# Optimization experiments

Measured on AMD Instinct MI355X. Metric: run time of the kernel, lower is better.

The kernel has to match this reference:

```python
import jax, jax.numpy as jnp
import numpy as np

B, S, K, N = 8, 8192, 1024, 1024  # batch, seq, in_features, out_features

def setup_inputs() -> dict:
    key = jax.random.key(0)
    k1, k2, k3, k4 = jax.random.split(key, 4)
    x = jax.random.normal(k1, (B, S, K), dtype=jnp.float32)
    # int8 codes stored as float (matches fp16 CB parameter in the module)
    CB = jnp.clip(jnp.round(jax.random.normal(k2, (N, K), dtype=jnp.float32) * 42.0), -127.0, 127.0)
    # per-output-channel absmax scales (positive)
    SCB = jax.random.uniform(k3, (N,), dtype=jnp.float32, minval=0.5, maxval=2.0)
    bias = jax.random.normal(k4, (N,), dtype=jnp.float32) * 0.02
    return {"x": x, "CB": CB, "SCB": SCB, "bias": bias}

def reference(x, CB, SCB, bias):
    # out = linear(x, CB) * (SCB/127) + bias  -- scale applied AFTER the GEMM,
    # exactly as in the non-BFA forward path of my_8bit_linear.
    out = jnp.einsum('bsk,nk->bsn', x, CB)        # [B, S, N]
    out = out * (SCB * (1.0 / 127.0)) + bias      # per-output-channel dequant + bias
    return out
```

## Files before the change

kernel.cpp:

```cpp
#include <hip/hip_runtime.h>

typedef _Float16 half8 __attribute__((ext_vector_type(8)));
typedef _Float16 half4 __attribute__((ext_vector_type(4)));
typedef float    f32x4 __attribute__((ext_vector_type(4)));

constexpr int Mtot = 65536, Ntot = 1024, Ktot = 1024;
constexpr int BM = 256, BN = 256, BK = 64;
constexpr int KT = Ktot / BK;
constexpr int MT = Mtot / BM;
constexpr int NT = Ntot / BN;

constexpr size_t XH_BYTES  = (size_t)MT * KT * 2 * 1024 * 16;
constexpr size_t CBH_BYTES = (size_t)NT * KT * 2 * 1024 * 16;

__global__ __launch_bounds__(256)
void cvt_pack(const float* __restrict__ src, _Float16* __restrict__ dst)
{
    const int C     = blockIdx.x * 256 + threadIdx.x;
    const int tile  = C >> 15;
    const int rem   = C & 32767;
    const int kt    = rem >> 11;
    const int kh    = (rem >> 10) & 1;
    const int off16 = rem & 1023;
    const int r     = off16 >> 2;
    const int hi    = (off16 & 3) ^ ((r >> 1) & 3);
    const float* s  = src + (size_t)(tile * 256 + r) * Ktot + kt * 64 + kh * 32 + hi * 8;
    f32x4 a = *(const f32x4*)s;
    f32x4 b = *(const f32x4*)(s + 4);
    half8 h = { (_Float16)a[0], (_Float16)a[1], (_Float16)a[2], (_Float16)a[3],
                (_Float16)b[0], (_Float16)b[1], (_Float16)b[2], (_Float16)b[3] };
    *(half8*)(dst + (size_t)C * 8) = h;
}

__global__ __launch_bounds__(512, 2)
void gemm8(const _Float16* __restrict__ Xh, const _Float16* __restrict__ CBh,
           const float* __restrict__ SCB,  const float* __restrict__ BIAS,
           float* __restrict__ OUT)
{
    __shared__ __align__(16) _Float16 lds[65536];

    const int nwg = gridDim.x;
    const int bid = blockIdx.x;
    const int wg  = (bid & 7) * (nwg >> 3) + (bid >> 3);
    const int nt  = wg & 3;
    const int mt  = wg >> 2;
    const int brow = mt * BM;
    const int bcol = nt * BN;

    const int tid  = threadIdx.x;
    const int lane = tid & 63;
    const int wid  = tid >> 6;
    const int wm   = wid >> 2;
    const int wn   = wid & 3;
    const int rA   = lane & 15;
    const int hi   = lane >> 4;
    const int sl   = hi ^ ((rA >> 1) & 3);

    const int aBaseH = (wm * 128 + rA) * 32 + sl * 8;
    const int bBaseH = 32768 + (wn * 64 + rA) * 32 + sl * 8;

    f32x4 acc[8][4];
#pragma unroll
    for (int m = 0; m < 8; ++m)
#pragma unroll
        for (int n = 0; n < 4; ++n)
            acc[m][n] = (f32x4)0.0f;

    auto stageA = [&](int kt, int kh, int buf) {
        const _Float16* sp = Xh + (size_t)((mt * KT + kt) * 2 + kh) * 8192;
#pragma unroll
        for (int g = 0; g < 2; ++g) {
            const int cell = g * 512 + tid;
            __builtin_amdgcn_global_load_lds(
                (const __attribute__((address_space(1))) void*)(sp + (size_t)cell * 8),
                (__attribute__((address_space(3))) void*)(&lds[buf * 16384 + kh * 8192 + cell * 8]),
                16, 0, 0);
        }
    };
    auto stageB = [&](int kt, int kh, int buf) {
        const _Float16* sp = CBh + (size_t)((nt * KT + kt) * 2 + kh) * 8192;
#pragma unroll
        for (int g = 0; g < 2; ++g) {
            const int cell = g * 512 + tid;
            __builtin_amdgcn_global_load_lds(
                (const __attribute__((address_space(1))) void*)(sp + (size_t)cell * 8),
                (__attribute__((address_space(3))) void*)(&lds[32768 + buf * 16384 + kh * 8192 + cell * 8]),
                16, 0, 0);
        }
    };

    auto phase = [&](int c, int ks, int mh, auto&& stageFn, int vm) {
        half8 af[4], bf[4];
        const int ab = c * 16384 + ks * 8192;
#pragma unroll
        for (int f = 0; f < 4; ++f)
            af[f] = *(const half8*)&lds[ab + aBaseH + mh * 2048 + f * 512];
#pragma unroll
        for (int n = 0; n < 4; ++n)
            bf[n] = *(const half8*)&lds[ab + bBaseH + n * 512];
        stageFn();
        __builtin_amdgcn_s_barrier();
        __builtin_amdgcn_s_setprio(1);
#pragma unroll
        for (int f = 0; f < 4; ++f)
#pragma unroll
            for (int n = 0; n < 4; ++n)
                acc[mh * 4 + f][n] = __builtin_amdgcn_mfma_f32_16x16x32_f16(
                    af[f], bf[n], acc[mh * 4 + f][n], 0, 0, 0);
        __builtin_amdgcn_s_setprio(0);
        if (vm == 4)      asm volatile("s_waitcnt vmcnt(4)" ::: "memory");
        else if (vm == 0) asm volatile("s_waitcnt vmcnt(0)" ::: "memory");
        __builtin_amdgcn_s_barrier();
        __builtin_amdgcn_sched_barrier(0);
    };

    stageA(0, 0, 0); stageB(0, 0, 0);
    stageA(0, 1, 0); stageB(0, 1, 0);
    asm volatile("s_waitcnt vmcnt(4)" ::: "memory");
    __builtin_amdgcn_s_barrier();
    __builtin_amdgcn_sched_barrier(0);

    for (int t = 0; t < KT - 1; ++t) {
        const int c = t & 1, nb = c ^ 1;
        phase(c, 0, 0, [&] { stageA(t + 1, 0, nb); }, -1);
        phase(c, 0, 1, [&] { stageB(t + 1, 0, nb); },  4);
        phase(c, 1, 0, [&] { stageA(t + 1, 1, nb); }, -1);
        phase(c, 1, 1, [&] { stageB(t + 1, 1, nb); },  4);
    }
    phase(1, 0, 0, [] {}, -1);
    phase(1, 0, 1, [] {},  0);
    phase(1, 1, 0, [] {}, -1);
    phase(1, 1, 1, [] {}, -1);

    const float inv127 = 1.0f / 127.0f;
#pragma unroll
    for (int n = 0; n < 4; ++n) {
        const int col = bcol + wn * 64 + n * 16 + rA;
        const float s  = SCB[col] * inv127;
        const float bb = BIAS[col];
#pragma unroll
        for (int m = 0; m < 8; ++m) {
            const int grow = brow + wm * 128 + m * 16 + (hi << 2);
            float* op = OUT + (size_t)grow * Ntot + col;
#pragma unroll
            for (int j = 0; j < 4; ++j)
                op[(size_t)j * Ntot] = acc[m][n][j] * s + bb;
        }
    }
}

namespace fb {
constexpr int BMf = 128, BNf = 128, BKf = 32;
constexpr int KTf = Ktot / BKf;
constexpr int LDK = 40;

__global__ __launch_bounds__(256, 2)
void gemm_fb(const float* __restrict__ X, const float* __restrict__ CB,
             const float* __restrict__ SCB, const float* __restrict__ BIAS,
             float* __restrict__ OUT)
{
    __shared__ _Float16 As[2][BMf][LDK];
    __shared__ _Float16 Bs[2][BNf][LDK];

    const int nwg = gridDim.x;
    const int bid = blockIdx.x;
    const int wg  = (bid & 7) * (nwg >> 3) + (bid >> 3);
    const int ntile = wg & 7;
    const int mtile = wg >> 3;
    const int brow = mtile * BMf;
    const int bcol = ntile * BNf;

    const int tid = threadIdx.x, lane = tid & 63, wid = tid >> 6;
    const int wm = wid >> 1, wn = wid & 1;
    const int c4 = tid & 7, r0 = tid >> 3;
    const float* aBase = X  + (size_t)(brow + r0) * Ktot + c4 * 4;
    const float* bBase = CB + (size_t)(bcol + r0) * Ktot + c4 * 4;

    f32x4 acc[4][4];
#pragma unroll
    for (int m = 0; m < 4; ++m)
#pragma unroll
        for (int n = 0; n < 4; ++n) acc[m][n] = (f32x4)0.0f;

    float4 arg[4], brg[4];
    auto loadTiles = [&](int t) {
#pragma unroll
        for (int s = 0; s < 4; ++s) {
            arg[s] = *(const float4*)(aBase + (size_t)s * 32 * Ktot + t * BKf);
            brg[s] = *(const float4*)(bBase + (size_t)s * 32 * Ktot + t * BKf);
        }
    };
    auto writeTiles = [&](int buf) {
#pragma unroll
        for (int s = 0; s < 4; ++s) {
            const int row = r0 + s * 32;
            half4 ha = { (_Float16)arg[s].x, (_Float16)arg[s].y,
                         (_Float16)arg[s].z, (_Float16)arg[s].w };
            half4 hb = { (_Float16)brg[s].x, (_Float16)brg[s].y,
                         (_Float16)brg[s].z, (_Float16)brg[s].w };
            *(half4*)&As[buf][row][c4 * 4] = ha;
            *(half4*)&Bs[buf][row][c4 * 4] = hb;
        }
    };

    loadTiles(0); writeTiles(0); loadTiles(1);
    __syncthreads();
    const int rA = lane & 15, ko = (lane >> 4) * 8;

    for (int t = 0; t < KTf; ++t) {
        const int cur = t & 1;
        if (t + 1 < KTf) writeTiles(cur ^ 1);
        if (t + 2 < KTf) loadTiles(t + 2);
        half8 af[4], bf[4];
#pragma unroll
        for (int m = 0; m < 4; ++m) af[m] = *(const half8*)&As[cur][wm * 64 + m * 16 + rA][ko];
#pragma unroll
        for (int n = 0; n < 4; ++n) bf[n] = *(const half8*)&Bs[cur][wn * 64 + n * 16 + rA][ko];
#pragma unroll
        for (int m = 0; m < 4; ++m)
#pragma unroll
            for (int n = 0; n < 4; ++n)
                acc[m][n] = __builtin_amdgcn_mfma_f32_16x16x32_f16(af[m], bf[n], acc[m][n], 0, 0, 0);
        __syncthreads();
    }

    const float inv127 = 1.0f / 127.0f;
#pragma unroll
    for (int n = 0; n < 4; ++n) {
        const int col = bcol + wn * 64 + n * 16 + rA;
        const float s = SCB[col] * inv127;
        const float bb = BIAS[col];
#pragma unroll
        for (int m = 0; m < 4; ++m) {
            const int grow = brow + wm * 64 + m * 16 + ((lane >> 4) << 2);
            float* op = OUT + (size_t)grow * Ntot + col;
#pragma unroll
            for (int j = 0; j < 4; ++j) op[(size_t)j * Ntot] = acc[m][n][j] * s + bb;
        }
    }
}
}

extern "C" void kernel_launch(void* const* d_in, const int* in_sizes, int n_in,
                              void* d_out, int out_size, void* d_ws, size_t ws_size,
                              hipStream_t stream) {
    const float* X    = (const float*)d_in[0];
    const float* CB   = (const float*)d_in[1];
    const float* SCB  = (const float*)d_in[2];
    const float* BIAS = (const float*)d_in[3];
    float* OUT = (float*)d_out;

    if (ws_size < XH_BYTES + CBH_BYTES) {
        fb::gemm_fb<<<dim3(4096), dim3(256), 0, stream>>>(X, CB, SCB, BIAS, OUT);
        return;
    }

    _Float16* Xh  = (_Float16*)d_ws;
    _Float16* CBh = (_Float16*)((char*)d_ws + XH_BYTES);

    cvt_pack<<<dim3(32768), dim3(256), 0, stream>>>(X, Xh);
    cvt_pack<<<dim3(512),   dim3(256), 0, stream>>>(CB, CBh);
    gemm8<<<dim3(MT * NT), dim3(512), 0, stream>>>(Xh, CBh, SCB, BIAS, OUT);
}
```

Before: 584.3 us.

## Deepen GEMM pipeline to 4-slot ring, reuse B fragments, coalesce cvt_pack reads

The GEMM's LDS staging changes from a double buffer of full K-tiles to a 4-slot ring of half-K slices, with three slices prefetched ahead, so there is more latency hiding between global loads and MFMA work. B fragments are now loaded once per K-slice and reused across both M halves, which cuts redundant LDS reads. The fp32→fp16 pack kernel now reads its source linearly and scatters the writes instead, so global reads are coalesced. The costs are tighter vmcnt bookkeeping, where a wrong wait count would give wrong results, and scattered writes in the pack kernel.

```diff
diff --git a/kernel.cpp b/kernel.cpp
--- a/kernel.cpp
+++ b/kernel.cpp
@@ -16,20 +16,22 @@
 __global__ __launch_bounds__(256)
 void cvt_pack(const float* __restrict__ src, _Float16* __restrict__ dst)
 {
-    const int C     = blockIdx.x * 256 + threadIdx.x;
-    const int tile  = C >> 15;
-    const int rem   = C & 32767;
-    const int kt    = rem >> 11;
-    const int kh    = (rem >> 10) & 1;
-    const int off16 = rem & 1023;
-    const int r     = off16 >> 2;
-    const int hi    = (off16 & 3) ^ ((r >> 1) & 3);
-    const float* s  = src + (size_t)(tile * 256 + r) * Ktot + kt * 64 + kh * 32 + hi * 8;
+    const int T = blockIdx.x * 256 + threadIdx.x;
+    const float* s = src + (size_t)T * 8;
     f32x4 a = *(const f32x4*)s;
     f32x4 b = *(const f32x4*)(s + 4);
     half8 h = { (_Float16)a[0], (_Float16)a[1], (_Float16)a[2], (_Float16)a[3],
                 (_Float16)b[0], (_Float16)b[1], (_Float16)b[2], (_Float16)b[3] };
-    *(half8*)(dst + (size_t)C * 8) = h;
+
+    const int g    = T >> 7;
+    const int k0   = (T & 127) << 3;
+    const int tile = g >> 8;
+    const int r    = g & 255;
+    const int kt   = k0 >> 6;
+    const int kh   = (k0 >> 5) & 1;
+    const int hi   = (k0 >> 3) & 3;
+    const int c    = r * 4 + (hi ^ ((r >> 1) & 3));
+    *(half8*)(dst + (size_t)((tile * KT + kt) * 2 + kh) * 8192 + (size_t)c * 8) = h;
 }
 
 __global__ __launch_bounds__(512, 2)
@@ -56,8 +58,8 @@
     const int hi   = lane >> 4;
     const int sl   = hi ^ ((rA >> 1) & 3);
 
-    const int aBaseH = (wm * 128 + rA) * 32 + sl * 8;
-    const int bBaseH = 32768 + (wn * 64 + rA) * 32 + sl * 8;
+    const int aOff = (wm * 128 + rA) * 32 + sl * 8;
+    const int bOff = (wn * 64  + rA) * 32 + sl * 8;
 
     f32x4 acc[8][4];
 #pragma unroll
@@ -66,38 +68,40 @@
         for (int n = 0; n < 4; ++n)
             acc[m][n] = (f32x4)0.0f;
 
-    auto stageA = [&](int kt, int kh, int buf) {
-        const _Float16* sp = Xh + (size_t)((mt * KT + kt) * 2 + kh) * 8192;
+    auto stageHalf = [&](int h) {
+        const int kt = h >> 1, kh = h & 1, slot = h & 3;
+        const _Float16* spA = Xh  + (size_t)((mt * KT + kt) * 2 + kh) * 8192;
+        const _Float16* spB = CBh + (size_t)((nt * KT + kt) * 2 + kh) * 8192;
 #pragma unroll
         for (int g = 0; g < 2; ++g) {
             const int cell = g * 512 + tid;
             __builtin_amdgcn_global_load_lds(
-                (const __attribute__((address_space(1))) void*)(sp + (size_t)cell * 8),
-                (__attribute__((address_space(3))) void*)(&lds[buf * 16384 + kh * 8192 + cell * 8]),
+                (const __attribute__((address_space(1))) void*)(spA + (size_t)cell * 8),
+                (__attribute__((address_space(3))) void*)(&lds[slot * 8192 + cell * 8]),
                 16, 0, 0);
         }
-    };
-    auto stageB = [&](int kt, int kh, int buf) {
-        const _Float16* sp = CBh + (size_t)((nt * KT + kt) * 2 + kh) * 8192;
 #pragma unroll
         for (int g = 0; g < 2; ++g) {
             const int cell = g * 512 + tid;
             __builtin_amdgcn_global_load_lds(
-                (const __attribute__((address_space(1))) void*)(sp + (size_t)cell * 8),
-                (__attribute__((address_space(3))) void*)(&lds[32768 + buf * 16384 + kh * 8192 + cell * 8]),
+                (const __attribute__((address_space(1))) void*)(spB + (size_t)cell * 8),
+                (__attribute__((address_space(3))) void*)(&lds[32768 + slot * 8192 + cell * 8]),
                 16, 0, 0);
         }
     };
 
-    auto phase = [&](int c, int ks, int mh, auto&& stageFn, int vm) {
-        half8 af[4], bf[4];
-        const int ab = c * 16384 + ks * 8192;
+    half8 bfk[4];
+    auto phase = [&](int slot, int mh, bool loadB, auto&& stageFn, int vm) {
+        half8 af[4];
+        const int ab = slot * 8192;
 #pragma unroll
         for (int f = 0; f < 4; ++f)
-            af[f] = *(const half8*)&lds[ab + aBaseH + mh * 2048 + f * 512];
-#pragma unroll
-        for (int n = 0; n < 4; ++n)
-            bf[n] = *(const half8*)&lds[ab + bBaseH + n * 512];
+            af[f] = *(const half8*)&lds[ab + aOff + mh * 2048 + f * 512];
+        if (loadB) {
+#pragma unroll
+            for (int n = 0; n < 4; ++n)
+                bfk[n] = *(const half8*)&lds[32768 + ab + bOff + n * 512];
+        }
         stageFn();
         __builtin_amdgcn_s_barrier();
         __builtin_amdgcn_s_setprio(1);
@@ -106,31 +110,35 @@
 #pragma unroll
             for (int n = 0; n < 4; ++n)
                 acc[mh * 4 + f][n] = __builtin_amdgcn_mfma_f32_16x16x32_f16(
-                    af[f], bf[n], acc[mh * 4 + f][n], 0, 0, 0);
+                    af[f], bfk[n], acc[mh * 4 + f][n], 0, 0, 0);
         __builtin_amdgcn_s_setprio(0);
-        if (vm == 4)      asm volatile("s_waitcnt vmcnt(4)" ::: "memory");
+        if (vm == 8)      asm volatile("s_waitcnt vmcnt(8)" ::: "memory");
+        else if (vm == 4) asm volatile("s_waitcnt vmcnt(4)" ::: "memory");
         else if (vm == 0) asm volatile("s_waitcnt vmcnt(0)" ::: "memory");
         __builtin_amdgcn_s_barrier();
         __builtin_amdgcn_sched_barrier(0);
     };
 
-    stageA(0, 0, 0); stageB(0, 0, 0);
-    stageA(0, 1, 0); stageB(0, 1, 0);
-    asm volatile("s_waitcnt vmcnt(4)" ::: "memory");
+    stageHalf(0); stageHalf(1); stageHalf(2);
+    asm volatile("s_waitcnt vmcnt(8)" ::: "memory");
     __builtin_amdgcn_s_barrier();
     __builtin_amdgcn_sched_barrier(0);
 
-    for (int t = 0; t < KT - 1; ++t) {
-        const int c = t & 1, nb = c ^ 1;
-        phase(c, 0, 0, [&] { stageA(t + 1, 0, nb); }, -1);
-        phase(c, 0, 1, [&] { stageB(t + 1, 0, nb); },  4);
-        phase(c, 1, 0, [&] { stageA(t + 1, 1, nb); }, -1);
-        phase(c, 1, 1, [&] { stageB(t + 1, 1, nb); },  4);
-    }
-    phase(1, 0, 0, [] {}, -1);
-    phase(1, 0, 1, [] {},  0);
-    phase(1, 1, 0, [] {}, -1);
-    phase(1, 1, 1, [] {}, -1);
+    for (int t = 0; t < KT - 2; ++t) {
+        const int s0 = (2 * t) & 3, s1 = (2 * t + 1) & 3;
+        phase(s0, 0, true,  [&] { stageHalf(2 * t + 3); }, -1);
+        phase(s0, 1, false, [] {},  8);
+        phase(s1, 0, true,  [&] { stageHalf(2 * t + 4); }, -1);
+        phase(s1, 1, false, [] {},  8);
+    }
+    phase(0, 0, true,  [&] { stageHalf(31); }, -1);
+    phase(0, 1, false, [] {}, 8);
+    phase(1, 0, true,  [] {}, -1);
+    phase(1, 1, false, [] {}, 4);
+    phase(2, 0, true,  [] {}, -1);
+    phase(2, 1, false, [] {}, 0);
+    phase(3, 0, true,  [] {}, -1);
+    phase(3, 1, false, [] {}, -1);
 
     const float inv127 = 1.0f / 127.0f;
 #pragma unroll
```

Result: no change. 584.1 us (-0.0%).
